# Performance work log

Measured on AMD Instinct MI355X. Metric: run time of the kernel, lower is better.

Reference implementation:

```python
import jax, jax.numpy as jnp
import numpy as np

HEAD_DIM = 1024
SCALE = HEAD_DIM ** -0.25  # qk_scale defaults to exponent -0.25


def setup_inputs() -> dict:
    key = jax.random.key(0)
    ks = jax.random.split(key, 6)
    B_s, B_q, C = 4096, 4096, 1024
    return {
        "query": jax.random.normal(ks[0], (B_q, C), dtype=jnp.float32),
        "s": jax.random.normal(ks[1], (B_s, C), dtype=jnp.float32),
        "TG_prompt": jax.random.normal(ks[2], (B_s, C), dtype=jnp.float32),
        "W_qkv": jax.random.normal(ks[3], (3 * HEAD_DIM, C), dtype=jnp.float32) * (C ** -0.5),
        "W_proj_s": jax.random.normal(ks[4], (HEAD_DIM, HEAD_DIM), dtype=jnp.float32) * (HEAD_DIM ** -0.5),
        "W_proj_q": jax.random.normal(ks[5], (HEAD_DIM, HEAD_DIM), dtype=jnp.float32) * (HEAD_DIM ** -0.5),
    }


def reference(query, s, TG_prompt, W_qkv, W_proj_s, W_proj_q):
    B_s = s.shape[0]
    t = s + TG_prompt                       # [B_s, C]
    c = jnp.concatenate([t, query], axis=0)  # [B, C], B = B_s + B_q
    x = c @ W_qkv.T                          # [B, 3*head_dim]
    q, k, v = jnp.split(x, 3, axis=-1)       # each [B, head_dim]
    # separate sqrt-scale on q and k, then full [B, B] scores
    attn = jax.nn.softmax((q * SCALE) @ (k.T * SCALE), axis=-1)
    attn_cq = attn[:B_s, B_s:]               # [B_s, B_q]
    attn_qc = attn[B_s:, :B_s]               # [B_q, B_s]
    # matmul against raw query / s (NOT v), then per-branch projection
    x_s = (attn_cq @ query) @ W_proj_s.T     # [B_s, head_dim]
    x_q = (attn_qc @ s) @ W_proj_q.T         # [B_q, head_dim]
    return (x_s, x_q)
```

## Files before the change

### kernel.cpp

```cpp
#include <hip/hip_runtime.h>


typedef unsigned short u16;
typedef __bf16 bf16x8 __attribute__((ext_vector_type(8)));
typedef float f32x4 __attribute__((ext_vector_type(4)));
typedef unsigned short u16x8 __attribute__((ext_vector_type(8)));

#define DEVI static __device__ __forceinline__

DEVI u16 f2b(float f) {
  unsigned int u = __float_as_uint(f);
  u += 0x7fffu + ((u >> 16) & 1u);
  return (u16)(u >> 16);
}


__global__ void prep_c(const float* __restrict__ query, const float* __restrict__ s,
                       const float* __restrict__ tg, u16* __restrict__ cB) {
  int base = (blockIdx.x * 256 + threadIdx.x) << 3;
  int row = base >> 10;
  u16x8 o;
  if (row < 4096) {
    float4 a0 = *(const float4*)(s + base);
    float4 a1 = *(const float4*)(s + base + 4);
    float4 b0 = *(const float4*)(tg + base);
    float4 b1 = *(const float4*)(tg + base + 4);
    o[0] = f2b(a0.x + b0.x); o[1] = f2b(a0.y + b0.y);
    o[2] = f2b(a0.z + b0.z); o[3] = f2b(a0.w + b0.w);
    o[4] = f2b(a1.x + b1.x); o[5] = f2b(a1.y + b1.y);
    o[6] = f2b(a1.z + b1.z); o[7] = f2b(a1.w + b1.w);
  } else {
    int qb = base - 4096 * 1024;
    float4 a0 = *(const float4*)(query + qb);
    float4 a1 = *(const float4*)(query + qb + 4);
    o[0] = f2b(a0.x); o[1] = f2b(a0.y); o[2] = f2b(a0.z); o[3] = f2b(a0.w);
    o[4] = f2b(a1.x); o[5] = f2b(a1.y); o[6] = f2b(a1.z); o[7] = f2b(a1.w);
  }
  *(u16x8*)(cB + base) = o;
}

__global__ void conv_bf16(const float* __restrict__ in, u16* __restrict__ out) {
  int base = (blockIdx.x * 256 + threadIdx.x) << 3;
  float4 a0 = *(const float4*)(in + base);
  float4 a1 = *(const float4*)(in + base + 4);
  u16x8 o;
  o[0] = f2b(a0.x); o[1] = f2b(a0.y); o[2] = f2b(a0.z); o[3] = f2b(a0.w);
  o[4] = f2b(a1.x); o[5] = f2b(a1.y); o[6] = f2b(a1.z); o[7] = f2b(a1.w);
  *(u16x8*)(out + base) = o;
}

__global__ void transpose_bf16(const float* __restrict__ in, u16* __restrict__ out,
                               int R, int C) {
  __shared__ float tile[32][33];
  int c0 = blockIdx.x * 32, r0 = blockIdx.y * 32;
  int tx = threadIdx.x, ty = threadIdx.y;
#pragma unroll
  for (int i = 0; i < 4; ++i)
    tile[ty + i * 8][tx] = in[(size_t)(r0 + ty + i * 8) * C + c0 + tx];
  __syncthreads();
#pragma unroll
  for (int i = 0; i < 4; ++i)
    out[(size_t)(c0 + ty + i * 8) * R + r0 + tx] = f2b(tile[tx][ty + i * 8]);
}


template <int EPI>
__global__ __launch_bounds__(256)
void gemm_bt(const u16* __restrict__ A, const u16* __restrict__ A1,
             const u16* __restrict__ B, const u16* __restrict__ B1,
             int lda, int ldb, int K, int ldc,
             u16* __restrict__ outb, u16* __restrict__ outb1,
             float* __restrict__ outf, float* __restrict__ outf1,
             float scale, const float* __restrict__ rs, const float* __restrict__ rs1,
             u16* __restrict__ Pcq, u16* __restrict__ Pqc,
             float* __restrict__ rowsum) {
  __shared__ __align__(16) u16 sA[128 * 64];
  __shared__ __align__(16) u16 sB[128 * 64];
  const int tid = threadIdx.x;
  const int lane = tid & 63;
  const int wave = tid >> 6;
  const int wr = (wave >> 1) * 64;
  const int wc = (wave & 1) * 64;
  const int ar = lane & 15;
  const int by = blockIdx.y, bx = blockIdx.x;
  const int z = (EPI == 2 || EPI == 3) ? blockIdx.z : 0;

  const u16* Ap = (z ? A1 : A);
  const u16* Bp = (z ? B1 : B);
  const u16* Ab = Ap + (size_t)(by * 128) * lda;
  const u16* Bb = Bp + (size_t)(bx * 128) * ldb;

  f32x4 zero = {0.0f, 0.0f, 0.0f, 0.0f};
  f32x4 acc[4][4];
#pragma unroll
  for (int i = 0; i < 4; ++i)
#pragma unroll
    for (int j = 0; j < 4; ++j) acc[i][j] = zero;

  const int sr = tid >> 3;
  const int scL = (tid & 7) << 3;
  const int scG = ((tid & 7) ^ (sr & 7)) << 3;

  for (int k0 = 0; k0 < K; k0 += 64) {
#pragma unroll
    for (int it = 0; it < 4; ++it) {
      int r = it * 32 + sr;
      __builtin_amdgcn_global_load_lds(
          (__attribute__((address_space(1))) void*)(Ab + (size_t)r * lda + k0 + scG),
          (__attribute__((address_space(3))) void*)(sA + r * 64 + scL), 16, 0, 0);
    }
#pragma unroll
    for (int it = 0; it < 4; ++it) {
      int r = it * 32 + sr;
      __builtin_amdgcn_global_load_lds(
          (__attribute__((address_space(1))) void*)(Bb + (size_t)r * ldb + k0 + scG),
          (__attribute__((address_space(3))) void*)(sB + r * 64 + scL), 16, 0, 0);
    }
    __syncthreads();
#pragma unroll
    for (int kk = 0; kk < 64; kk += 32) {
      const int gl = (kk >> 3) + (lane >> 4);
      bf16x8 af[4], bfr[4];
#pragma unroll
      for (int t = 0; t < 4; ++t) {
        const int row = wr + t * 16 + ar;
        af[t] = *(const bf16x8*)(sA + row * 64 + ((gl ^ (row & 7)) << 3));
      }
#pragma unroll
      for (int t = 0; t < 4; ++t) {
        const int row = wc + t * 16 + ar;
        bfr[t] = *(const bf16x8*)(sB + row * 64 + ((gl ^ (row & 7)) << 3));
      }
#pragma unroll
      for (int tm = 0; tm < 4; ++tm)
#pragma unroll
        for (int tn = 0; tn < 4; ++tn)
          acc[tm][tn] = __builtin_amdgcn_mfma_f32_16x16x32_bf16(
              af[tm], bfr[tn], acc[tm][tn], 0, 0, 0);
    }
    __syncthreads();
  }

  const int qr = (lane >> 4) * 4;
  const int qc = lane & 15;

  if constexpr (EPI == 0) {
#pragma unroll
    for (int tm = 0; tm < 4; ++tm)
#pragma unroll
      for (int r = 0; r < 4; ++r) {
        int row = by * 128 + wr + tm * 16 + qr + r;
#pragma unroll
        for (int tn = 0; tn < 4; ++tn) {
          int col = bx * 128 + wc + tn * 16 + qc;
          outb[(size_t)row * ldc + col] = f2b(acc[tm][tn][r] * scale);
        }
      }
  } else if constexpr (EPI == 1) {
    const bool top = (by < 32);
    const bool left = (bx < 32);
    u16* pdst = nullptr;
    if (top && !left) pdst = Pcq;
    if (!top && left) pdst = Pqc;
    const int rofs = top ? 0 : 4096;
    const int cofs = left ? 0 : 4096;
#pragma unroll
    for (int tm = 0; tm < 4; ++tm) {
      float rsum[4] = {0.f, 0.f, 0.f, 0.f};
#pragma unroll
      for (int tn = 0; tn < 4; ++tn) {
        float e[4];
#pragma unroll
        for (int r = 0; r < 4; ++r) {
          e[r] = __expf(acc[tm][tn][r]);
          rsum[r] += e[r];
        }
        if (pdst) {
          int col = bx * 128 + wc + tn * 16 + qc - cofs;
#pragma unroll
          for (int r = 0; r < 4; ++r) {
            int row = by * 128 + wr + tm * 16 + qr + r - rofs;
            pdst[(size_t)row * 4096 + col] = f2b(e[r]);
          }
        }
      }
#pragma unroll
      for (int r = 0; r < 4; ++r) {
        float v = rsum[r];
        v += __shfl_xor(v, 1);
        v += __shfl_xor(v, 2);
        v += __shfl_xor(v, 4);
        v += __shfl_xor(v, 8);
        if ((lane & 15) == 0)
          atomicAdd(&rowsum[by * 128 + wr + tm * 16 + qr + r], v);
      }
    }
  } else if constexpr (EPI == 2) {
    u16* ob = z ? outb1 : outb;
    const float* rsz = z ? rs1 : rs;
#pragma unroll
    for (int tm = 0; tm < 4; ++tm)
#pragma unroll
      for (int r = 0; r < 4; ++r) {
        int row = by * 128 + wr + tm * 16 + qr + r;
        float inv = 1.0f / rsz[row];
#pragma unroll
        for (int tn = 0; tn < 4; ++tn) {
          int col = bx * 128 + wc + tn * 16 + qc;
          ob[(size_t)row * ldc + col] = f2b(acc[tm][tn][r] * inv);
        }
      }
  } else {
    float* of = z ? outf1 : outf;
#pragma unroll
    for (int tm = 0; tm < 4; ++tm)
#pragma unroll
      for (int r = 0; r < 4; ++r) {
        int row = by * 128 + wr + tm * 16 + qr + r;
#pragma unroll
        for (int tn = 0; tn < 4; ++tn) {
          int col = bx * 128 + wc + tn * 16 + qc;
          of[(size_t)row * ldc + col] = acc[tm][tn][r];
        }
      }
  }
}


extern "C" void kernel_launch(void* const* d_in, const int* in_sizes, int n_in,
                              void* d_out, int out_size, void* d_ws, size_t ws_size,
                              hipStream_t stream) {
  (void)in_sizes; (void)n_in; (void)out_size; (void)ws_size;
  const float* query = (const float*)d_in[0];
  const float* s     = (const float*)d_in[1];
  const float* tg    = (const float*)d_in[2];
  const float* Wqkv  = (const float*)d_in[3];
  const float* Wps   = (const float*)d_in[4];
  const float* Wpq   = (const float*)d_in[5];
  float* out = (float*)d_out;

  char* ws = (char*)d_ws;
  u16* cB     = (u16*)ws; ws += (size_t)8192 * 1024 * 2;
  u16* qks    = (u16*)ws; ws += (size_t)8192 * 2048 * 2;
  u16* queryT = (u16*)ws; ws += (size_t)1024 * 4096 * 2;
  u16* sT     = (u16*)ws; ws += (size_t)1024 * 4096 * 2;
  u16* WqkB   = (u16*)ws; ws += (size_t)2048 * 1024 * 2;
  u16* WpsB   = (u16*)ws; ws += (size_t)1024 * 1024 * 2;
  u16* WpqB   = (u16*)ws; ws += (size_t)1024 * 1024 * 2;
  u16* Pcq    = (u16*)ws; ws += (size_t)4096 * 4096 * 2;
  u16* Pqc    = (u16*)ws; ws += (size_t)4096 * 4096 * 2;
  u16* Ys     = (u16*)ws; ws += (size_t)4096 * 1024 * 2;
  u16* Yq     = (u16*)ws; ws += (size_t)4096 * 1024 * 2;
  float* rowsum = (float*)ws;

  const float SCALE = 0.17677669529663687f;

  (void)hipMemsetAsync(rowsum, 0, 8192 * sizeof(float), stream);
  prep_c<<<4096, 256, 0, stream>>>(query, s, tg, cB);
  conv_bf16<<<1024, 256, 0, stream>>>(Wqkv, WqkB);
  conv_bf16<<<512, 256, 0, stream>>>(Wps, WpsB);
  conv_bf16<<<512, 256, 0, stream>>>(Wpq, WpqB);
  transpose_bf16<<<dim3(32, 128), dim3(32, 8), 0, stream>>>(query, queryT, 4096, 1024);
  transpose_bf16<<<dim3(32, 128), dim3(32, 8), 0, stream>>>(s, sT, 4096, 1024);

  gemm_bt<0><<<dim3(16, 64), 256, 0, stream>>>(
      cB, nullptr, WqkB, nullptr, 1024, 1024, 1024, 2048,
      qks, nullptr, nullptr, nullptr, SCALE, nullptr, nullptr,
      nullptr, nullptr, nullptr);
  gemm_bt<1><<<dim3(64, 64), 256, 0, stream>>>(
      qks, nullptr, qks + 1024, nullptr, 2048, 2048, 1024, 0,
      nullptr, nullptr, nullptr, nullptr, 0.f, nullptr, nullptr,
      Pcq, Pqc, rowsum);
  gemm_bt<2><<<dim3(8, 32, 2), 256, 0, stream>>>(
      Pcq, Pqc, queryT, sT, 4096, 4096, 4096, 1024,
      Ys, Yq, nullptr, nullptr, 0.f, rowsum, rowsum + 4096,
      nullptr, nullptr, nullptr);
  gemm_bt<3><<<dim3(8, 32, 2), 256, 0, stream>>>(
      Ys, Yq, WpsB, WpqB, 1024, 1024, 1024, 1024,
      nullptr, nullptr, out, out + (size_t)4096 * 1024, 0.f, nullptr, nullptr,
      nullptr, nullptr, nullptr);
}
```

Baseline: 485.6 us.

## Use 256x128 tiles for QK GEMMs, fold log2e into q, merge prep launches

Adds a gemm_big kernel with 512 threads and 256x128 output tiles for the QKV projection and score GEMMs, which halves the number of blocks and increases operand reuse per block. The log2(e) factor is folded into the q scale so the softmax epilogue can use the hardware v_exp_f32 instruction directly instead of __expf. The three weight conversions are merged into one launch, and the two transposes into another, to cut launch overhead. The larger tiles raise LDS and register pressure, which may lower occupancy, and the unnormalized exp still has no max subtraction.

```diff
diff --git a/kernel.cpp b/kernel.cpp
--- a/kernel.cpp
+++ b/kernel.cpp
@@ -12,6 +12,12 @@
   unsigned int u = __float_as_uint(f);
   u += 0x7fffu + ((u >> 16) & 1u);
   return (u16)(u >> 16);
+}
+
+DEVI float exp2_hw(float x) {
+  float r;
+  asm("v_exp_f32 %0, %1" : "=v"(r) : "v"(x));
+  return r;
 }
 
 
@@ -39,8 +45,15 @@
   *(u16x8*)(cB + base) = o;
 }
 
-__global__ void conv_bf16(const float* __restrict__ in, u16* __restrict__ out) {
-  int base = (blockIdx.x * 256 + threadIdx.x) << 3;
+__global__ void conv3(const float* __restrict__ w0, const float* __restrict__ w1,
+                      const float* __restrict__ w2, u16* __restrict__ o0,
+                      u16* __restrict__ o1, u16* __restrict__ o2) {
+  int b = blockIdx.x;
+  const float* in; u16* out; int lb;
+  if (b < 1024)      { in = w0; out = o0; lb = b; }
+  else if (b < 1536) { in = w1; out = o1; lb = b - 1024; }
+  else               { in = w2; out = o2; lb = b - 1536; }
+  int base = (lb * 256 + threadIdx.x) << 3;
   float4 a0 = *(const float4*)(in + base);
   float4 a1 = *(const float4*)(in + base + 4);
   u16x8 o;
@@ -49,18 +62,150 @@
   *(u16x8*)(out + base) = o;
 }
 
-__global__ void transpose_bf16(const float* __restrict__ in, u16* __restrict__ out,
-                               int R, int C) {
+__global__ void transpose2(const float* __restrict__ query, const float* __restrict__ s,
+                           u16* __restrict__ queryT, u16* __restrict__ sT) {
   __shared__ float tile[32][33];
+  const float* in = blockIdx.z ? s : query;
+  u16* out = blockIdx.z ? sT : queryT;
   int c0 = blockIdx.x * 32, r0 = blockIdx.y * 32;
   int tx = threadIdx.x, ty = threadIdx.y;
 #pragma unroll
   for (int i = 0; i < 4; ++i)
-    tile[ty + i * 8][tx] = in[(size_t)(r0 + ty + i * 8) * C + c0 + tx];
+    tile[ty + i * 8][tx] = in[(size_t)(r0 + ty + i * 8) * 1024 + c0 + tx];
   __syncthreads();
 #pragma unroll
   for (int i = 0; i < 4; ++i)
-    out[(size_t)(c0 + ty + i * 8) * R + r0 + tx] = f2b(tile[tx][ty + i * 8]);
+    out[(size_t)(c0 + ty + i * 8) * 4096 + r0 + tx] = f2b(tile[tx][ty + i * 8]);
+}
+
+
+template <int EPI>
+__global__ __launch_bounds__(512, 6)
+void gemm_big(const u16* __restrict__ A, const u16* __restrict__ B,
+              int lda, int ldb, int K, int ldc,
+              u16* __restrict__ outb, float sq, float sk,
+              u16* __restrict__ Pcq, u16* __restrict__ Pqc,
+              float* __restrict__ rowsum) {
+  __shared__ __align__(16) u16 sA[256 * 64];
+  __shared__ __align__(16) u16 sB[128 * 64];
+  const int tid = threadIdx.x;
+  const int lane = tid & 63;
+  const int wave = tid >> 6;
+  const int wr = (wave >> 1) * 64;
+  const int wc = (wave & 1) * 64;
+  const int ar = lane & 15;
+  const int by = blockIdx.y, bx = blockIdx.x;
+
+  const u16* Ab = A + (size_t)(by * 256) * lda;
+  const u16* Bb = B + (size_t)(bx * 128) * ldb;
+
+  f32x4 zero = {0.0f, 0.0f, 0.0f, 0.0f};
+  f32x4 acc[4][4];
+#pragma unroll
+  for (int i = 0; i < 4; ++i)
+#pragma unroll
+    for (int j = 0; j < 4; ++j) acc[i][j] = zero;
+
+  const int sr = tid >> 3;
+  const int scL = (tid & 7) << 3;
+  const int scG = ((tid & 7) ^ (sr & 7)) << 3;
+
+  for (int k0 = 0; k0 < K; k0 += 64) {
+#pragma unroll
+    for (int it = 0; it < 4; ++it) {
+      int r = it * 64 + sr;
+      __builtin_amdgcn_global_load_lds(
+          (__attribute__((address_space(1))) void*)(Ab + (size_t)r * lda + k0 + scG),
+          (__attribute__((address_space(3))) void*)(sA + r * 64 + scL), 16, 0, 0);
+    }
+#pragma unroll
+    for (int it = 0; it < 2; ++it) {
+      int r = it * 64 + sr;
+      __builtin_amdgcn_global_load_lds(
+          (__attribute__((address_space(1))) void*)(Bb + (size_t)r * ldb + k0 + scG),
+          (__attribute__((address_space(3))) void*)(sB + r * 64 + scL), 16, 0, 0);
+    }
+    __syncthreads();
+#pragma unroll
+    for (int kk = 0; kk < 64; kk += 32) {
+      const int gl = (kk >> 3) + (lane >> 4);
+      bf16x8 af[4], bfr[4];
+#pragma unroll
+      for (int t = 0; t < 4; ++t) {
+        const int row = wr + t * 16 + ar;
+        af[t] = *(const bf16x8*)(sA + row * 64 + ((gl ^ (row & 7)) << 3));
+      }
+#pragma unroll
+      for (int t = 0; t < 4; ++t) {
+        const int row = wc + t * 16 + ar;
+        bfr[t] = *(const bf16x8*)(sB + row * 64 + ((gl ^ (row & 7)) << 3));
+      }
+#pragma unroll
+      for (int tm = 0; tm < 4; ++tm)
+#pragma unroll
+        for (int tn = 0; tn < 4; ++tn)
+          acc[tm][tn] = __builtin_amdgcn_mfma_f32_16x16x32_bf16(
+              af[tm], bfr[tn], acc[tm][tn], 0, 0, 0);
+    }
+    __syncthreads();
+  }
+
+  const int qr = (lane >> 4) * 4;
+  const int qc = lane & 15;
+
+  if constexpr (EPI == 0) {
+#pragma unroll
+    for (int tm = 0; tm < 4; ++tm)
+#pragma unroll
+      for (int r = 0; r < 4; ++r) {
+        int row = by * 256 + wr + tm * 16 + qr + r;
+#pragma unroll
+        for (int tn = 0; tn < 4; ++tn) {
+          int col = bx * 128 + wc + tn * 16 + qc;
+          float sc = (col < 1024) ? sq : sk;
+          outb[(size_t)row * ldc + col] = f2b(acc[tm][tn][r] * sc);
+        }
+      }
+  } else {
+    const bool top = (by < 16);
+    const bool left = (bx < 32);
+    u16* pdst = nullptr;
+    if (top && !left) pdst = Pcq;
+    if (!top && left) pdst = Pqc;
+    const int rofs = top ? 0 : 4096;
+    const int cofs = left ? 0 : 4096;
+#pragma unroll
+    for (int tm = 0; tm < 4; ++tm) {
+      float rsum[4] = {0.f, 0.f, 0.f, 0.f};
+#pragma unroll
+      for (int tn = 0; tn < 4; ++tn) {
+        float e[4];
+#pragma unroll
+        for (int r = 0; r < 4; ++r) {
+          e[r] = exp2_hw(acc[tm][tn][r]);
+          rsum[r] += e[r];
+        }
+        if (pdst) {
+          int col = bx * 128 + wc + tn * 16 + qc - cofs;
+#pragma unroll
+          for (int r = 0; r < 4; ++r) {
+            int row = by * 256 + wr + tm * 16 + qr + r - rofs;
+            pdst[(size_t)row * 4096 + col] = f2b(e[r]);
+          }
+        }
+      }
+#pragma unroll
+      for (int r = 0; r < 4; ++r) {
+        float v = rsum[r];
+        v += __shfl_xor(v, 1);
+        v += __shfl_xor(v, 2);
+        v += __shfl_xor(v, 4);
+        v += __shfl_xor(v, 8);
+        if ((lane & 15) == 0)
+          atomicAdd(&rowsum[by * 256 + wr + tm * 16 + qr + r], v);
+      }
+    }
+  }
 }
 
 
@@ -71,9 +216,7 @@
              int lda, int ldb, int K, int ldc,
              u16* __restrict__ outb, u16* __restrict__ outb1,
              float* __restrict__ outf, float* __restrict__ outf1,
-             float scale, const float* __restrict__ rs, const float* __restrict__ rs1,
-             u16* __restrict__ Pcq, u16* __restrict__ Pqc,
-             float* __restrict__ rowsum) {
+             const float* __restrict__ rs, const float* __restrict__ rs1) {
   __shared__ __align__(16) u16 sA[128 * 64];
   __shared__ __align__(16) u16 sB[128 * 64];
   const int tid = threadIdx.x;
@@ -83,12 +226,10 @@
   const int wc = (wave & 1) * 64;
   const int ar = lane & 15;
   const int by = blockIdx.y, bx = blockIdx.x;
-  const int z = (EPI == 2 || EPI == 3) ? blockIdx.z : 0;
-
-  const u16* Ap = (z ? A1 : A);
-  const u16* Bp = (z ? B1 : B);
-  const u16* Ab = Ap + (size_t)(by * 128) * lda;
-  const u16* Bb = Bp + (size_t)(bx * 128) * ldb;
+  const int z = blockIdx.z;
+
+  const u16* Ab = (z ? A1 : A) + (size_t)(by * 128) * lda;
+  const u16* Bb = (z ? B1 : B) + (size_t)(bx * 128) * ldb;
 
   f32x4 zero = {0.0f, 0.0f, 0.0f, 0.0f};
   f32x4 acc[4][4];
@@ -144,58 +285,7 @@
   const int qr = (lane >> 4) * 4;
   const int qc = lane & 15;
 
-  if constexpr (EPI == 0) {
-#pragma unroll
-    for (int tm = 0; tm < 4; ++tm)
-#pragma unroll
-      for (int r = 0; r < 4; ++r) {
-        int row = by * 128 + wr + tm * 16 + qr + r;
-#pragma unroll
-        for (int tn = 0; tn < 4; ++tn) {
-          int col = bx * 128 + wc + tn * 16 + qc;
-          outb[(size_t)row * ldc + col] = f2b(acc[tm][tn][r] * scale);
-        }
-      }
-  } else if constexpr (EPI == 1) {
-    const bool top = (by < 32);
-    const bool left = (bx < 32);
-    u16* pdst = nullptr;
-    if (top && !left) pdst = Pcq;
-    if (!top && left) pdst = Pqc;
-    const int rofs = top ? 0 : 4096;
-    const int cofs = left ? 0 : 4096;
-#pragma unroll
-    for (int tm = 0; tm < 4; ++tm) {
-      float rsum[4] = {0.f, 0.f, 0.f, 0.f};
-#pragma unroll
-      for (int tn = 0; tn < 4; ++tn) {
-        float e[4];
-#pragma unroll
-        for (int r = 0; r < 4; ++r) {
-          e[r] = __expf(acc[tm][tn][r]);
-          rsum[r] += e[r];
-        }
-        if (pdst) {
-          int col = bx * 128 + wc + tn * 16 + qc - cofs;
-#pragma unroll
-          for (int r = 0; r < 4; ++r) {
-            int row = by * 128 + wr + tm * 16 + qr + r - rofs;
-            pdst[(size_t)row * 4096 + col] = f2b(e[r]);
-          }
-        }
-      }
-#pragma unroll
-      for (int r = 0; r < 4; ++r) {
-        float v = rsum[r];
-        v += __shfl_xor(v, 1);
-        v += __shfl_xor(v, 2);
-        v += __shfl_xor(v, 4);
-        v += __shfl_xor(v, 8);
-        if ((lane & 15) == 0)
-          atomicAdd(&rowsum[by * 128 + wr + tm * 16 + qr + r], v);
-      }
-    }
-  } else if constexpr (EPI == 2) {
+  if constexpr (EPI == 2) {
     u16* ob = z ? outb1 : outb;
     const float* rsz = z ? rs1 : rs;
 #pragma unroll
@@ -254,29 +344,23 @@
   float* rowsum = (float*)ws;
 
   const float SCALE = 0.17677669529663687f;
+  const float LOG2E = 1.4426950408889634f;
 
   (void)hipMemsetAsync(rowsum, 0, 8192 * sizeof(float), stream);
   prep_c<<<4096, 256, 0, stream>>>(query, s, tg, cB);
-  conv_bf16<<<1024, 256, 0, stream>>>(Wqkv, WqkB);
-  conv_bf16<<<512, 256, 0, stream>>>(Wps, WpsB);
-  conv_bf16<<<512, 256, 0, stream>>>(Wpq, WpqB);
-  transpose_bf16<<<dim3(32, 128), dim3(32, 8), 0, stream>>>(query, queryT, 4096, 1024);
-  transpose_bf16<<<dim3(32, 128), dim3(32, 8), 0, stream>>>(s, sT, 4096, 1024);
-
-  gemm_bt<0><<<dim3(16, 64), 256, 0, stream>>>(
-      cB, nullptr, WqkB, nullptr, 1024, 1024, 1024, 2048,
-      qks, nullptr, nullptr, nullptr, SCALE, nullptr, nullptr,
-      nullptr, nullptr, nullptr);
-  gemm_bt<1><<<dim3(64, 64), 256, 0, stream>>>(
-      qks, nullptr, qks + 1024, nullptr, 2048, 2048, 1024, 0,
-      nullptr, nullptr, nullptr, nullptr, 0.f, nullptr, nullptr,
-      Pcq, Pqc, rowsum);
+  conv3<<<2048, 256, 0, stream>>>(Wqkv, Wps, Wpq, WqkB, WpsB, WpqB);
+  transpose2<<<dim3(32, 128, 2), dim3(32, 8), 0, stream>>>(query, s, queryT, sT);
+
+  gemm_big<0><<<dim3(16, 32), 512, 0, stream>>>(
+      cB, WqkB, 1024, 1024, 1024, 2048,
+      qks, SCALE * LOG2E, SCALE, nullptr, nullptr, nullptr);
+  gemm_big<1><<<dim3(64, 32), 512, 0, stream>>>(
+      qks, qks + 1024, 2048, 2048, 1024, 0,
+      nullptr, 0.f, 0.f, Pcq, Pqc, rowsum);
   gemm_bt<2><<<dim3(8, 32, 2), 256, 0, stream>>>(
       Pcq, Pqc, queryT, sT, 4096, 4096, 4096, 1024,
-      Ys, Yq, nullptr, nullptr, 0.f, rowsum, rowsum + 4096,
-      nullptr, nullptr, nullptr);
+      Ys, Yq, nullptr, nullptr, rowsum, rowsum + 4096);
   gemm_bt<3><<<dim3(8, 32, 2), 256, 0, stream>>>(
       Ys, Yq, WpsB, WpqB, 1024, 1024, 1024, 1024,
-      nullptr, nullptr, out, out + (size_t)4096 * 1024, 0.f, nullptr, nullptr,
-      nullptr, nullptr, nullptr);
-}
+      nullptr, nullptr, out, out + (size_t)4096 * 1024, nullptr, nullptr);
+}
```

Result: slower. 1.591 ms (+227.7%).
